# Optimization experiments

Hardware: AMD Instinct MI355X
Metric: run time of the kernel (lower is better)

Reference implementation:

```python
import jax, jax.numpy as jnp
import numpy as np

N_ROWS = 262144
FEAT = 1024
N_CORES = 4096
SEG = N_ROWS // N_CORES
H1 = H2 = H3 = 1024
NUM_CLASSES = 2
BN_EPS = 1e-5


def setup_inputs() -> dict:
    key = jax.random.key(0)
    ks = jax.random.split(key, 12)
    x = jax.random.normal(ks[0], (N_ROWS, FEAT), dtype=jnp.float32)
    # equal-length segments: start indices 0, SEG, 2*SEG, ...
    corelen = (jnp.arange(N_CORES) * SEG).astype(jnp.int64)
    def lin(k, din, dout):
        kw, kb = jax.random.split(k)
        W = jax.random.normal(kw, (din, dout), dtype=jnp.float32) / np.sqrt(din)
        b = jnp.zeros((dout,), dtype=jnp.float32)
        return W, b
    W1, b1 = lin(ks[1], FEAT, H1)
    W2, b2 = lin(ks[2], H1, H2)
    W3, b3 = lin(ks[3], H2, H3)
    W4, b4 = lin(ks[4], H3, NUM_CLASSES)
    g1 = jnp.ones((H1,), jnp.float32); be1 = jnp.zeros((H1,), jnp.float32)
    g2 = jnp.ones((H2,), jnp.float32); be2 = jnp.zeros((H2,), jnp.float32)
    g3 = jnp.ones((H3,), jnp.float32); be3 = jnp.zeros((H3,), jnp.float32)
    return {"x": x, "corelen": corelen,
            "W1": W1, "b1": b1, "g1": g1, "be1": be1,
            "W2": W2, "b2": b2, "g2": g2, "be2": be2,
            "W3": W3, "b3": b3, "g3": g3, "be3": be3,
            "W4": W4, "b4": b4}


def _batchnorm(h, g, b):
    # BatchNorm1d, training mode: biased batch statistics over the batch dim
    m = jnp.mean(h, axis=0)
    v = jnp.mean(jnp.square(h - m), axis=0)
    return g * (h - m) * jax.lax.rsqrt(v + BN_EPS) + b


def reference(x, corelen, W1, b1, g1, be1, W2, b2, g2, be2, W3, b3, g3, be3, W4, b4):
    n = x.shape[0]
    # segment id of row r = number of starts <= r, minus 1 (rows before
    # corelen[0] get id -1 and are dropped, matching the torch loop)
    seg_ids = jnp.searchsorted(corelen, jnp.arange(n), side="right") - 1
    agg = jax.ops.segment_sum(x, seg_ids, num_segments=corelen.shape[0])  # [C, FEAT]
    h = jax.nn.relu(_batchnorm(agg @ W1 + b1, g1, be1))
    h = jax.nn.relu(_batchnorm(h @ W2 + b2, g2, be2))
    h = jax.nn.relu(_batchnorm(h @ W3 + b3, g3, be3))
    return h @ W4 + b4  # [C, NUM_CLASSES]
```

## Files before the change

### kernel.cpp

```cpp
#include <hip/hip_runtime.h>
#include <hip/hip_bf16.h>
#include <stdint.h>

#define N_ROWS 262144
#define FEAT 1024
#define N_CORES 4096
#define HDIM 1024
#define BN_EPS 1e-5f

typedef __attribute__((ext_vector_type(8))) short bf16x8;
typedef __attribute__((ext_vector_type(8))) unsigned short u16x8;
typedef __attribute__((ext_vector_type(4))) float f32x4;

__device__ __forceinline__ unsigned short f2bf(float f) {
  __hip_bfloat16 h = __float2bfloat16(f);
  return __builtin_bit_cast(unsigned short, h);
}
__device__ __forceinline__ float bf2f(unsigned short u) {
  unsigned int x = ((unsigned int)u) << 16;
  return __builtin_bit_cast(float, x);
}

__device__ __forceinline__ void gll16(const unsigned short* g, unsigned short* l) {
  __builtin_amdgcn_global_load_lds(
      (const __attribute__((address_space(1))) void*)g,
      (__attribute__((address_space(3))) void*)l, 16, 0, 0);
}

__global__ __launch_bounds__(256)
void k_segsum(const float* __restrict__ x, const int* __restrict__ corelen,
              unsigned short* __restrict__ aggb) {
  const int seg = blockIdx.x;
  const int t = threadIdx.x;
  const int start = corelen[seg];
  const int end = (seg + 1 < N_CORES) ? corelen[seg + 1] : N_ROWS;
  float4 a0 = make_float4(0.f, 0.f, 0.f, 0.f);
  float4 a1 = make_float4(0.f, 0.f, 0.f, 0.f);
  const float* xp = x + (size_t)start * FEAT + t * 4;
  int r = start;
  for (; r + 2 <= end; r += 2) {
    const float4 v0 = *(const float4*)xp;
    const float4 v1 = *(const float4*)(xp + FEAT);
    a0.x += v0.x; a0.y += v0.y; a0.z += v0.z; a0.w += v0.w;
    a1.x += v1.x; a1.y += v1.y; a1.z += v1.z; a1.w += v1.w;
    xp += 2 * FEAT;
  }
  if (r < end) {
    const float4 v0 = *(const float4*)xp;
    a0.x += v0.x; a0.y += v0.y; a0.z += v0.z; a0.w += v0.w;
  }
  a0.x += a1.x; a0.y += a1.y; a0.z += a1.z; a0.w += a1.w;
  ushort4 o;
  o.x = f2bf(a0.x); o.y = f2bf(a0.y); o.z = f2bf(a0.z); o.w = f2bf(a0.w);
  *(ushort4*)(aggb + (size_t)seg * FEAT + t * 4) = o;
}

__global__ __launch_bounds__(256)
void k_transpose_all(const float* __restrict__ W1, const float* __restrict__ W2,
                     const float* __restrict__ W3, unsigned short* __restrict__ Wt) {
  __shared__ unsigned short tile[32][33];
  const int l = blockIdx.z;
  const float* W = (l == 0) ? W1 : (l == 1) ? W2 : W3;
  unsigned short* Wo = Wt + (size_t)l * HDIM * HDIM;
  const int tx = threadIdx.x, ty = threadIdx.y;
  const int n0 = blockIdx.x * 32, k0 = blockIdx.y * 32;
#pragma unroll
  for (int i = 0; i < 4; ++i)
    tile[ty + 8 * i][tx] = f2bf(W[(size_t)(k0 + ty + 8 * i) * HDIM + n0 + tx]);
  __syncthreads();
#pragma unroll
  for (int i = 0; i < 4; ++i)
    Wo[(size_t)(n0 + ty + 8 * i) * HDIM + k0 + tx] = tile[tx][ty + 8 * i];
}

#define BM 128
#define BN 64
#define BK 64
#define NT (HDIM / BK)
__global__ __launch_bounds__(256)
void k_gemm_bt(const unsigned short* __restrict__ A,
               const unsigned short* __restrict__ Bt,
               const float* __restrict__ bias,
               unsigned short* __restrict__ C,
               float* __restrict__ sums, float* __restrict__ sumsq) {
  __shared__ unsigned short As[2][BM * BK];
  __shared__ unsigned short Bs[2][BN * BK];
  const int t = threadIdx.x;
  const int lane = t & 63;
  const int w = t >> 6;
  const int tileM = blockIdx.x * BM;
  const int tileN = blockIdx.y * BN;
  const int wr = (w >> 1) * 64;
  const int wc = (w & 1) * 32;
  const int fr = lane & 15;
  const int kk = (lane >> 4) * 8;
  const int lr = lane >> 3;
  const int sc = ((lane & 7) * 8) ^ (lr << 3);

  const unsigned short* pA = A + (size_t)(tileM + w * 32 + lr) * HDIM + sc;
  const unsigned short* pB = Bt + (size_t)(tileN + w * 16 + lr) * HDIM + sc;

  f32x4 acc[4][2] = {};

#define STAGE(buf, k0)                                                   \
  {                                                                      \
    _Pragma("unroll") for (int j = 0; j < 4; ++j)                        \
        gll16(pA + (k0) + j * 8 * HDIM, &As[buf][(w * 32 + j * 8) * BK]);\
    _Pragma("unroll") for (int j = 0; j < 2; ++j)                        \
        gll16(pB + (k0) + j * 8 * HDIM, &Bs[buf][(w * 16 + j * 8) * BK]);\
  }

  STAGE(0, 0);
  __syncthreads();
  for (int kt = 0; kt < NT; ++kt) {
    const int cur = kt & 1;
    if (kt < NT - 1) STAGE(cur ^ 1, (kt + 1) * BK);
#pragma unroll
    for (int ks = 0; ks < 2; ++ks) {
      const int pc = (ks * 32 + kk) ^ ((fr & 7) << 3);
      bf16x8 af[4], bfv[2];
#pragma unroll
      for (int m = 0; m < 4; ++m)
        af[m] = *(const bf16x8*)&As[cur][(wr + m * 16 + fr) * BK + pc];
#pragma unroll
      for (int n = 0; n < 2; ++n)
        bfv[n] = *(const bf16x8*)&Bs[cur][(wc + n * 16 + fr) * BK + pc];
#pragma unroll
      for (int m = 0; m < 4; ++m)
#pragma unroll
        for (int n = 0; n < 2; ++n)
          acc[m][n] = __builtin_amdgcn_mfma_f32_16x16x32_bf16(af[m], bfv[n], acc[m][n], 0, 0, 0);
    }
    __syncthreads();
  }
#undef STAGE

  const int cr = (lane >> 4) * 4;
  const int cc = lane & 15;
#pragma unroll
  for (int n = 0; n < 2; ++n) {
    const int col = tileN + wc + n * 16 + cc;
    const float bv = bias[col];
    float s = 0.f, s2 = 0.f;
#pragma unroll
    for (int m = 0; m < 4; ++m) {
      unsigned short* cp = C + (size_t)(tileM + wr + m * 16 + cr) * HDIM + col;
#pragma unroll
      for (int j = 0; j < 4; ++j) {
        const float h = acc[m][n][j] + bv;
        cp[(size_t)j * HDIM] = f2bf(h);
        s += h; s2 += h * h;
      }
    }
    s  += __shfl_xor(s, 16, 64);  s  += __shfl_xor(s, 32, 64);
    s2 += __shfl_xor(s2, 16, 64); s2 += __shfl_xor(s2, 32, 64);
    if ((lane >> 4) == 0) {
      atomicAdd(&sums[col], s);
      atomicAdd(&sumsq[col], s2);
    }
  }
}

__global__ __launch_bounds__(256)
void k_finalize(const float* __restrict__ sums, const float* __restrict__ sumsq,
                const float* __restrict__ g, const float* __restrict__ be,
                float* __restrict__ scale, float* __restrict__ shift) {
  const int c = blockIdx.x * 256 + threadIdx.x;
  const float mean = sums[c] * (1.f / N_CORES);
  const float var = sumsq[c] * (1.f / N_CORES) - mean * mean;
  const float sc = g[c] * rsqrtf(var + BN_EPS);
  scale[c] = sc;
  shift[c] = be[c] - mean * sc;
}

__global__ __launch_bounds__(256)
void k_norm_relu(const unsigned short* __restrict__ Hb, const float* __restrict__ scale,
                 const float* __restrict__ shift, unsigned short* __restrict__ Ab) {
  const size_t i8 = ((size_t)blockIdx.x * 256 + threadIdx.x) * 8;
  const u16x8 v = *(const u16x8*)(Hb + i8);
  const int c = (int)(i8 & (HDIM - 1));
  const float4 sc0 = *(const float4*)(scale + c);
  const float4 sc1 = *(const float4*)(scale + c + 4);
  const float4 sh0 = *(const float4*)(shift + c);
  const float4 sh1 = *(const float4*)(shift + c + 4);
  u16x8 o;
  o[0] = f2bf(fmaxf(bf2f(v[0]) * sc0.x + sh0.x, 0.f));
  o[1] = f2bf(fmaxf(bf2f(v[1]) * sc0.y + sh0.y, 0.f));
  o[2] = f2bf(fmaxf(bf2f(v[2]) * sc0.z + sh0.z, 0.f));
  o[3] = f2bf(fmaxf(bf2f(v[3]) * sc0.w + sh0.w, 0.f));
  o[4] = f2bf(fmaxf(bf2f(v[4]) * sc1.x + sh1.x, 0.f));
  o[5] = f2bf(fmaxf(bf2f(v[5]) * sc1.y + sh1.y, 0.f));
  o[6] = f2bf(fmaxf(bf2f(v[6]) * sc1.z + sh1.z, 0.f));
  o[7] = f2bf(fmaxf(bf2f(v[7]) * sc1.w + sh1.w, 0.f));
  *(u16x8*)(Ab + i8) = o;
}

__global__ __launch_bounds__(256)
void k_final(const unsigned short* __restrict__ Ab, const float* __restrict__ W4,
             const float* __restrict__ b4, float* __restrict__ out) {
  const int t = threadIdx.x;
  const int w = t >> 6, lane = t & 63;
  const int row = blockIdx.x * 4 + w;
  const unsigned short* a = Ab + (size_t)row * HDIM + lane * 16;
  const bf16x8 v0 = *(const bf16x8*)a;
  const bf16x8 v1 = *(const bf16x8*)(a + 8);
  float s0 = 0.f, s1 = 0.f;
  const int kbase = lane * 16;
#pragma unroll
  for (int j = 0; j < 8; ++j) {
    const float av = bf2f((unsigned short)v0[j]);
    s0 += av * W4[(kbase + j) * 2 + 0];
    s1 += av * W4[(kbase + j) * 2 + 1];
  }
#pragma unroll
  for (int j = 0; j < 8; ++j) {
    const float av = bf2f((unsigned short)v1[j]);
    s0 += av * W4[(kbase + 8 + j) * 2 + 0];
    s1 += av * W4[(kbase + 8 + j) * 2 + 1];
  }
#pragma unroll
  for (int off = 32; off >= 1; off >>= 1) {
    s0 += __shfl_down(s0, off, 64);
    s1 += __shfl_down(s1, off, 64);
  }
  if (lane == 0) {
    out[row * 2 + 0] = s0 + b4[0];
    out[row * 2 + 1] = s1 + b4[1];
  }
}

extern "C" void kernel_launch(void* const* d_in, const int* in_sizes, int n_in,
                              void* d_out, int out_size, void* d_ws, size_t ws_size,
                              hipStream_t stream) {
  (void)in_sizes; (void)n_in; (void)out_size; (void)ws_size;
  const float* x       = (const float*)d_in[0];
  const int* corelen   = (const int*)d_in[1];
  const float* W1  = (const float*)d_in[2];
  const float* b1  = (const float*)d_in[3];
  const float* g1  = (const float*)d_in[4];
  const float* be1 = (const float*)d_in[5];
  const float* W2  = (const float*)d_in[6];
  const float* b2  = (const float*)d_in[7];
  const float* g2  = (const float*)d_in[8];
  const float* be2 = (const float*)d_in[9];
  const float* W3  = (const float*)d_in[10];
  const float* b3  = (const float*)d_in[11];
  const float* g3  = (const float*)d_in[12];
  const float* be3 = (const float*)d_in[13];
  const float* W4  = (const float*)d_in[14];
  const float* b4  = (const float*)d_in[15];
  float* out = (float*)d_out;

  char* ws = (char*)d_ws;
  unsigned short* Hb   = (unsigned short*)(ws);
  unsigned short* Abf  = (unsigned short*)(ws + (8u << 20));
  unsigned short* Wt   = (unsigned short*)(ws + (16u << 20));
  float* stats = (float*)(ws + (22u << 20));
  float* scale = stats + 6 * HDIM;
  float* shift = scale + HDIM;

  hipMemsetAsync(stats, 0, 6 * HDIM * sizeof(float), stream);
  k_transpose_all<<<dim3(32, 32, 3), dim3(32, 8), 0, stream>>>(W1, W2, W3, Wt);
  k_segsum<<<N_CORES, 256, 0, stream>>>(x, corelen, Abf);

  const float* bs[3]  = {b1, b2, b3};
  const float* gs[3]  = {g1, g2, g3};
  const float* bes[3] = {be1, be2, be3};
  for (int l = 0; l < 3; ++l) {
    float* sums  = stats + l * 2 * HDIM;
    float* sumsq = sums + HDIM;
    k_gemm_bt<<<dim3(N_CORES / BM, HDIM / BN), 256, 0, stream>>>(
        Abf, Wt + (size_t)l * HDIM * HDIM, bs[l], Hb, sums, sumsq);
    k_finalize<<<HDIM / 256, 256, 0, stream>>>(sums, sumsq, gs[l], bes[l], scale, shift);
    k_norm_relu<<<(N_CORES * HDIM / 8) / 256, 256, 0, stream>>>(Hb, scale, shift, Abf);
  }
  k_final<<<N_CORES / 4, 256, 0, stream>>>(Abf, W4, b4, out);
}
```

Measured before the change: 312.1 us.

## Triple-buffer GEMM LDS staging with fine-grained vmcnt waits

```diff
diff --git a/kernel.cpp b/kernel.cpp
--- a/kernel.cpp
+++ b/kernel.cpp
@@ -83,8 +83,8 @@
                const float* __restrict__ bias,
                unsigned short* __restrict__ C,
                float* __restrict__ sums, float* __restrict__ sumsq) {
-  __shared__ unsigned short As[2][BM * BK];
-  __shared__ unsigned short Bs[2][BN * BK];
+  __shared__ unsigned short As[3][BM * BK];
+  __shared__ unsigned short Bs[3][BN * BK];
   const int t = threadIdx.x;
   const int lane = t & 63;
   const int w = t >> 6;
@@ -102,37 +102,58 @@
 
   f32x4 acc[4][2] = {};
 
-#define STAGE(buf, k0)                                                   \
-  {                                                                      \
-    _Pragma("unroll") for (int j = 0; j < 4; ++j)                        \
-        gll16(pA + (k0) + j * 8 * HDIM, &As[buf][(w * 32 + j * 8) * BK]);\
-    _Pragma("unroll") for (int j = 0; j < 2; ++j)                        \
-        gll16(pB + (k0) + j * 8 * HDIM, &Bs[buf][(w * 16 + j * 8) * BK]);\
-  }
+#define STAGE(buf, k0)                                                     \
+  do {                                                                     \
+    _Pragma("unroll") for (int j = 0; j < 4; ++j)                          \
+        gll16(pA + (k0) + j * 8 * HDIM, &As[buf][(w * 32 + j * 8) * BK]);  \
+    _Pragma("unroll") for (int j = 0; j < 2; ++j)                          \
+        gll16(pB + (k0) + j * 8 * HDIM, &Bs[buf][(w * 16 + j * 8) * BK]);  \
+  } while (0)
+
+#define COMPUTE(buf)                                                       \
+  do {                                                                     \
+    _Pragma("unroll") for (int ks = 0; ks < 2; ++ks) {                     \
+      const int pc = (ks * 32 + kk) ^ ((fr & 7) << 3);                     \
+      bf16x8 af[4], bfv[2];                                                \
+      _Pragma("unroll") for (int m = 0; m < 4; ++m)                        \
+          af[m] = *(const bf16x8*)&As[buf][(wr + m * 16 + fr) * BK + pc];  \
+      _Pragma("unroll") for (int n = 0; n < 2; ++n)                        \
+          bfv[n] = *(const bf16x8*)&Bs[buf][(wc + n * 16 + fr) * BK + pc]; \
+      _Pragma("unroll") for (int m = 0; m < 4; ++m)                        \
+          _Pragma("unroll") for (int n = 0; n < 2; ++n)                    \
+              acc[m][n] = __builtin_amdgcn_mfma_f32_16x16x32_bf16(         \
+                  af[m], bfv[n], acc[m][n], 0, 0, 0);                      \
+    }                                                                      \
+  } while (0)
+
+#define STEP(b, tt)                                                        \
+  do {                                                                     \
+    if ((tt) + 2 < NT) STAGE(((b) + 2) % 3, ((tt) + 2) * BK);              \
+    COMPUTE(b);                                                            \
+    asm volatile("s_waitcnt lgkmcnt(0)" ::: "memory");                     \
+    __builtin_amdgcn_sched_barrier(0);                                     \
+    if ((tt) + 1 < NT) {                                                   \
+      if ((tt) + 2 < NT)                                                   \
+        asm volatile("s_waitcnt vmcnt(6)" ::: "memory");                   \
+      else                                                                 \
+        asm volatile("s_waitcnt vmcnt(0)" ::: "memory");                   \
+      __builtin_amdgcn_s_barrier();                                        \
+      __builtin_amdgcn_sched_barrier(0);                                   \
+    }                                                                      \
+  } while (0)
 
   STAGE(0, 0);
-  __syncthreads();
-  for (int kt = 0; kt < NT; ++kt) {
-    const int cur = kt & 1;
-    if (kt < NT - 1) STAGE(cur ^ 1, (kt + 1) * BK);
-#pragma unroll
-    for (int ks = 0; ks < 2; ++ks) {
-      const int pc = (ks * 32 + kk) ^ ((fr & 7) << 3);
-      bf16x8 af[4], bfv[2];
-#pragma unroll
-      for (int m = 0; m < 4; ++m)
-        af[m] = *(const bf16x8*)&As[cur][(wr + m * 16 + fr) * BK + pc];
-#pragma unroll
-      for (int n = 0; n < 2; ++n)
-        bfv[n] = *(const bf16x8*)&Bs[cur][(wc + n * 16 + fr) * BK + pc];
-#pragma unroll
-      for (int m = 0; m < 4; ++m)
-#pragma unroll
-        for (int n = 0; n < 2; ++n)
-          acc[m][n] = __builtin_amdgcn_mfma_f32_16x16x32_bf16(af[m], bfv[n], acc[m][n], 0, 0, 0);
-    }
-    __syncthreads();
-  }
+  STAGE(1, BK);
+  asm volatile("s_waitcnt vmcnt(6)" ::: "memory");
+  __builtin_amdgcn_s_barrier();
+  __builtin_amdgcn_sched_barrier(0);
+  for (int kt = 0; kt < NT; kt += 3) {
+    STEP(0, kt);
+    if (kt + 1 < NT) STEP(1, kt + 1);
+    if (kt + 2 < NT) STEP(2, kt + 2);
+  }
+#undef STEP
+#undef COMPUTE
 #undef STAGE
 
   const int cr = (lane >> 4) * 4;
```

After: 313.0 us. About the same (+0.3%).

## Fuse BN finalize into norm/final kernels and use 8 waves per GEMM block

Applied to the files above, without the earlier changes.

```diff
diff --git a/kernel.cpp b/kernel.cpp
--- a/kernel.cpp
+++ b/kernel.cpp
@@ -77,7 +77,7 @@
 #define BN 64
 #define BK 64
 #define NT (HDIM / BK)
-__global__ __launch_bounds__(256)
+__global__ __launch_bounds__(512)
 void k_gemm_bt(const unsigned short* __restrict__ A,
                const unsigned short* __restrict__ Bt,
                const float* __restrict__ bias,
@@ -87,28 +87,27 @@
   __shared__ unsigned short Bs[2][BN * BK];
   const int t = threadIdx.x;
   const int lane = t & 63;
-  const int w = t >> 6;
+  const int wv = t >> 6;
   const int tileM = blockIdx.x * BM;
   const int tileN = blockIdx.y * BN;
-  const int wr = (w >> 1) * 64;
-  const int wc = (w & 1) * 32;
+  const int wr = (wv >> 1) * 32;
+  const int wc = (wv & 1) * 32;
   const int fr = lane & 15;
   const int kk = (lane >> 4) * 8;
   const int lr = lane >> 3;
   const int sc = ((lane & 7) * 8) ^ (lr << 3);
 
-  const unsigned short* pA = A + (size_t)(tileM + w * 32 + lr) * HDIM + sc;
-  const unsigned short* pB = Bt + (size_t)(tileN + w * 16 + lr) * HDIM + sc;
-
-  f32x4 acc[4][2] = {};
-
-#define STAGE(buf, k0)                                                   \
-  {                                                                      \
-    _Pragma("unroll") for (int j = 0; j < 4; ++j)                        \
-        gll16(pA + (k0) + j * 8 * HDIM, &As[buf][(w * 32 + j * 8) * BK]);\
-    _Pragma("unroll") for (int j = 0; j < 2; ++j)                        \
-        gll16(pB + (k0) + j * 8 * HDIM, &Bs[buf][(w * 16 + j * 8) * BK]);\
-  }
+  const unsigned short* pA = A + (size_t)(tileM + wv * 8 + lr) * HDIM + sc;
+  const unsigned short* pB = Bt + (size_t)(tileN + wv * 8 + lr) * HDIM + sc;
+
+  f32x4 acc[2][2] = {};
+
+#define STAGE(buf, k0)                                                     \
+  do {                                                                     \
+    gll16(pA + (k0), &As[buf][(wv * 8) * BK]);                             \
+    gll16(pA + (k0) + 64 * HDIM, &As[buf][(64 + wv * 8) * BK]);            \
+    gll16(pB + (k0), &Bs[buf][(wv * 8) * BK]);                             \
+  } while (0)
 
   STAGE(0, 0);
   __syncthreads();
@@ -118,15 +117,15 @@
 #pragma unroll
     for (int ks = 0; ks < 2; ++ks) {
       const int pc = (ks * 32 + kk) ^ ((fr & 7) << 3);
-      bf16x8 af[4], bfv[2];
-#pragma unroll
-      for (int m = 0; m < 4; ++m)
+      bf16x8 af[2], bfv[2];
+#pragma unroll
+      for (int m = 0; m < 2; ++m)
         af[m] = *(const bf16x8*)&As[cur][(wr + m * 16 + fr) * BK + pc];
 #pragma unroll
       for (int n = 0; n < 2; ++n)
         bfv[n] = *(const bf16x8*)&Bs[cur][(wc + n * 16 + fr) * BK + pc];
 #pragma unroll
-      for (int m = 0; m < 4; ++m)
+      for (int m = 0; m < 2; ++m)
 #pragma unroll
         for (int n = 0; n < 2; ++n)
           acc[m][n] = __builtin_amdgcn_mfma_f32_16x16x32_bf16(af[m], bfv[n], acc[m][n], 0, 0, 0);
@@ -143,7 +142,7 @@
     const float bv = bias[col];
     float s = 0.f, s2 = 0.f;
 #pragma unroll
-    for (int m = 0; m < 4; ++m) {
+    for (int m = 0; m < 2; ++m) {
       unsigned short* cp = C + (size_t)(tileM + wr + m * 16 + cr) * HDIM + col;
 #pragma unroll
       for (int j = 0; j < 4; ++j) {
@@ -162,61 +161,47 @@
 }
 
 __global__ __launch_bounds__(256)
-void k_finalize(const float* __restrict__ sums, const float* __restrict__ sumsq,
-                const float* __restrict__ g, const float* __restrict__ be,
-                float* __restrict__ scale, float* __restrict__ shift) {
-  const int c = blockIdx.x * 256 + threadIdx.x;
-  const float mean = sums[c] * (1.f / N_CORES);
-  const float var = sumsq[c] * (1.f / N_CORES) - mean * mean;
-  const float sc = g[c] * rsqrtf(var + BN_EPS);
-  scale[c] = sc;
-  shift[c] = be[c] - mean * sc;
-}
-
-__global__ __launch_bounds__(256)
-void k_norm_relu(const unsigned short* __restrict__ Hb, const float* __restrict__ scale,
-                 const float* __restrict__ shift, unsigned short* __restrict__ Ab) {
+void k_norm_relu(const unsigned short* __restrict__ Hb,
+                 const float* __restrict__ sums, const float* __restrict__ sumsq,
+                 const float* __restrict__ g, const float* __restrict__ be,
+                 unsigned short* __restrict__ Ab) {
   const size_t i8 = ((size_t)blockIdx.x * 256 + threadIdx.x) * 8;
   const u16x8 v = *(const u16x8*)(Hb + i8);
   const int c = (int)(i8 & (HDIM - 1));
-  const float4 sc0 = *(const float4*)(scale + c);
-  const float4 sc1 = *(const float4*)(scale + c + 4);
-  const float4 sh0 = *(const float4*)(shift + c);
-  const float4 sh1 = *(const float4*)(shift + c + 4);
   u16x8 o;
-  o[0] = f2bf(fmaxf(bf2f(v[0]) * sc0.x + sh0.x, 0.f));
-  o[1] = f2bf(fmaxf(bf2f(v[1]) * sc0.y + sh0.y, 0.f));
-  o[2] = f2bf(fmaxf(bf2f(v[2]) * sc0.z + sh0.z, 0.f));
-  o[3] = f2bf(fmaxf(bf2f(v[3]) * sc0.w + sh0.w, 0.f));
-  o[4] = f2bf(fmaxf(bf2f(v[4]) * sc1.x + sh1.x, 0.f));
-  o[5] = f2bf(fmaxf(bf2f(v[5]) * sc1.y + sh1.y, 0.f));
-  o[6] = f2bf(fmaxf(bf2f(v[6]) * sc1.z + sh1.z, 0.f));
-  o[7] = f2bf(fmaxf(bf2f(v[7]) * sc1.w + sh1.w, 0.f));
+#pragma unroll
+  for (int j = 0; j < 8; ++j) {
+    const float mean = sums[c + j] * (1.f / N_CORES);
+    const float var = sumsq[c + j] * (1.f / N_CORES) - mean * mean;
+    const float sc = g[c + j] * rsqrtf(var + BN_EPS);
+    const float sh = be[c + j] - mean * sc;
+    o[j] = f2bf(fmaxf(bf2f(v[j]) * sc + sh, 0.f));
+  }
   *(u16x8*)(Ab + i8) = o;
 }
 
 __global__ __launch_bounds__(256)
-void k_final(const unsigned short* __restrict__ Ab, const float* __restrict__ W4,
-             const float* __restrict__ b4, float* __restrict__ out) {
+void k_final(const unsigned short* __restrict__ Hb,
+             const float* __restrict__ sums, const float* __restrict__ sumsq,
+             const float* __restrict__ g, const float* __restrict__ be,
+             const float* __restrict__ W4, const float* __restrict__ b4,
+             float* __restrict__ out) {
   const int t = threadIdx.x;
   const int w = t >> 6, lane = t & 63;
   const int row = blockIdx.x * 4 + w;
-  const unsigned short* a = Ab + (size_t)row * HDIM + lane * 16;
-  const bf16x8 v0 = *(const bf16x8*)a;
-  const bf16x8 v1 = *(const bf16x8*)(a + 8);
+  const int kbase = lane * 16;
+  const unsigned short* a = Hb + (size_t)row * HDIM + kbase;
   float s0 = 0.f, s1 = 0.f;
-  const int kbase = lane * 16;
-#pragma unroll
-  for (int j = 0; j < 8; ++j) {
-    const float av = bf2f((unsigned short)v0[j]);
-    s0 += av * W4[(kbase + j) * 2 + 0];
-    s1 += av * W4[(kbase + j) * 2 + 1];
-  }
-#pragma unroll
-  for (int j = 0; j < 8; ++j) {
-    const float av = bf2f((unsigned short)v1[j]);
-    s0 += av * W4[(kbase + 8 + j) * 2 + 0];
-    s1 += av * W4[(kbase + 8 + j) * 2 + 1];
+#pragma unroll
+  for (int j = 0; j < 16; ++j) {
+    const int col = kbase + j;
+    const float mean = sums[col] * (1.f / N_CORES);
+    const float var = sumsq[col] * (1.f / N_CORES) - mean * mean;
+    const float sc = g[col] * rsqrtf(var + BN_EPS);
+    const float sh = be[col] - mean * sc;
+    const float av = fmaxf(bf2f(a[j]) * sc + sh, 0.f);
+    s0 += av * W4[col * 2 + 0];
+    s1 += av * W4[col * 2 + 1];
   }
 #pragma unroll
   for (int off = 32; off >= 1; off >>= 1) {
@@ -256,8 +241,6 @@
   unsigned short* Abf  = (unsigned short*)(ws + (8u << 20));
   unsigned short* Wt   = (unsigned short*)(ws + (16u << 20));
   float* stats = (float*)(ws + (22u << 20));
-  float* scale = stats + 6 * HDIM;
-  float* shift = scale + HDIM;
 
   hipMemsetAsync(stats, 0, 6 * HDIM * sizeof(float), stream);
   k_transpose_all<<<dim3(32, 32, 3), dim3(32, 8), 0, stream>>>(W1, W2, W3, Wt);
@@ -269,10 +252,13 @@
   for (int l = 0; l < 3; ++l) {
     float* sums  = stats + l * 2 * HDIM;
     float* sumsq = sums + HDIM;
-    k_gemm_bt<<<dim3(N_CORES / BM, HDIM / BN), 256, 0, stream>>>(
+    k_gemm_bt<<<dim3(N_CORES / BM, HDIM / BN), 512, 0, stream>>>(
         Abf, Wt + (size_t)l * HDIM * HDIM, bs[l], Hb, sums, sumsq);
-    k_finalize<<<HDIM / 256, 256, 0, stream>>>(sums, sumsq, gs[l], bes[l], scale, shift);
-    k_norm_relu<<<(N_CORES * HDIM / 8) / 256, 256, 0, stream>>>(Hb, scale, shift, Abf);
-  }
-  k_final<<<N_CORES / 4, 256, 0, stream>>>(Abf, W4, b4, out);
-}
+    if (l < 2)
+      k_norm_relu<<<(N_CORES * HDIM / 8) / 256, 256, 0, stream>>>(
+          Hb, sums, sumsq, gs[l], bes[l], Abf);
+    else
+      k_final<<<N_CORES / 4, 256, 0, stream>>>(
+          Hb, sums, sumsq, gs[l], bes[l], W4, b4, out);
+  }
+}
```

Result: faster. 302.3 us (-3.1%).
